# Kernel optimization log

Hardware: AMD Instinct MI355X
Metric: run time of the kernel (lower is better)

## Reference

```python
import jax, jax.numpy as jnp
import numpy as np

DIM = 512
HEADS = 8
DIM_HEAD = 64
INNER = HEADS * DIM_HEAD  # 512
NARROW_K = 9
WIDE_K = 9
WIDE_DIL = 5


def setup_inputs() -> dict:
    key = jax.random.key(0)
    ks = jax.random.split(key, 12)
    b, n = 4, 2048
    s = lambda fan_in: 1.0 / np.sqrt(fan_in)
    inp = {
        'tokens': jax.random.normal(ks[0], (b, n, DIM), jnp.float32),
        'mask': jax.random.randint(ks[1], (b, n), 0, 2) > 0,
        'w_qkv': jax.random.normal(ks[2], (DIM, INNER * 3), jnp.float32) * s(DIM),
        'w_out': jax.random.normal(ks[3], (INNER, DIM), jnp.float32) * s(INNER),
        'b_out': jnp.zeros((DIM,), jnp.float32),
        'w_narrow': jax.random.normal(ks[4], (DIM, DIM, NARROW_K), jnp.float32) * s(DIM * NARROW_K),
        'b_narrow': jnp.zeros((DIM,), jnp.float32),
        'w_wide': jax.random.normal(ks[5], (DIM, DIM, WIDE_K), jnp.float32) * s(DIM * WIDE_K),
        'b_wide': jnp.zeros((DIM,), jnp.float32),
        'ln1_g': jnp.ones((DIM,), jnp.float32),
        'ln1_b': jnp.zeros((DIM,), jnp.float32),
        'ff_w': jax.random.normal(ks[6], (DIM, DIM), jnp.float32) * s(DIM),
        'ff_b': jnp.zeros((DIM,), jnp.float32),
        'ln2_g': jnp.ones((DIM,), jnp.float32),
        'ln2_b': jnp.zeros((DIM,), jnp.float32),
    }
    return inp


def layer_norm(x, g, b, eps=1e-5):
    m = jnp.mean(x, axis=-1, keepdims=True)
    v = jnp.mean(jnp.square(x - m), axis=-1, keepdims=True)
    return (x - m) / jnp.sqrt(v + eps) * g + b


def rope_encoding(seq_len, dim_head, dtype):
    inv_freq = 1.0 / (10000.0 ** (jnp.arange(0, dim_head, 2, dtype=jnp.float32) / dim_head))
    pos = jnp.arange(seq_len, dtype=jnp.float32)
    sinu = jnp.einsum('i,j->ij', pos, inv_freq)  # [n, d/2]
    return jnp.concatenate([jnp.sin(sinu), jnp.cos(sinu)], axis=-1).astype(dtype)  # [n, d]


def attn(tokens, mask, w_qkv, w_out, b_out):
    b, n, _ = tokens.shape
    qkv = tokens @ w_qkv  # [b, n, 3*inner]
    q, k, v = jnp.split(qkv, 3, axis=-1)
    reshp = lambda t: t.reshape(b, n, HEADS, DIM_HEAD).transpose(0, 2, 1, 3)  # b h n d
    q, k, v = reshp(q), reshp(k), reshp(v)
    rope = rope_encoding(n, DIM_HEAD, tokens.dtype)  # [n, d]
    q = q + rope
    k = k + rope
    mask4 = mask[:, None, :, None]  # b 1 n 1
    big = jnp.finfo(k.dtype).max
    k = jnp.where(mask4, k, -big)
    q = jax.nn.softmax(q, axis=-1) * (DIM_HEAD ** -0.5)
    k = jax.nn.softmax(k, axis=2)  # over n
    v = jnp.where(mask4, v, 0.0)
    context = jnp.einsum('bhnd,bhne->bhde', k, v)
    out = jnp.einsum('bhde,bhnd->bhne', context, q)
    out = out.transpose(0, 2, 1, 3).reshape(b, n, INNER)
    return out @ w_out + b_out


def conv1d(x, w, b, padding, dilation):
    # x: [b, c, n], w: [out, in, k]
    y = jax.lax.conv_general_dilated(
        x, w, window_strides=(1,), padding=[(padding, padding)],
        rhs_dilation=(dilation,), dimension_numbers=('NCW', 'OIW', 'NCW'))
    return y + b[None, :, None]


def reference(tokens, mask, w_qkv, w_out, b_out, w_narrow, b_narrow,
              w_wide, b_wide, ln1_g, ln1_b, ff_w, ff_b, ln2_g, ln2_b):
    tokens = attn(tokens, mask, w_qkv, w_out, b_out)
    conv_in = tokens.transpose(0, 2, 1)  # b d n
    conv_in = jnp.where(mask[:, None, :], conv_in, 0.0)
    narrow = jax.nn.gelu(conv1d(conv_in, w_narrow, b_narrow, NARROW_K // 2, 1), approximate=False)
    wide_pad = (WIDE_K + (WIDE_K - 1) * (WIDE_DIL - 1)) // 2  # 20
    wide = jax.nn.gelu(conv1d(conv_in, w_wide, b_wide, wide_pad, WIDE_DIL), approximate=False)
    tokens = tokens + narrow.transpose(0, 2, 1) + wide.transpose(0, 2, 1)
    tokens = layer_norm(tokens, ln1_g, ln1_b)
    tokens = layer_norm(jax.nn.gelu(tokens @ ff_w + ff_b, approximate=False), ln2_g, ln2_b)
    return tokens
```

## Files before the change

### kernel.cpp

```cpp
#include <hip/hip_runtime.h>
#include <hip/hip_bf16.h>

#define BB 4
#define NN 2048
#define NROWS (BB*NN)

typedef unsigned short u16;
typedef __bf16 bf16x8 __attribute__((ext_vector_type(8)));
typedef u16    u16x8  __attribute__((ext_vector_type(8)));
typedef float  fx4    __attribute__((ext_vector_type(4)));

__device__ __forceinline__ float bf2f(u16 u){
  union { float f; unsigned int i; } x; x.i = ((unsigned int)u) << 16; return x.f;
}
__device__ __forceinline__ u16 f2bf(float f){
  union { float f; unsigned int i; } x; x.f = f;
  unsigned int i = x.i;
  i += 0x7fffu + ((i >> 16) & 1u);
  return (u16)(i >> 16);
}
__device__ __forceinline__ float geluf(float x){
  return 0.5f * x * (1.0f + erff(x * 0.70710678118654752f));
}

__global__ __launch_bounds__(256) void sniff_k(const u16* tokens, const unsigned int* mask, int* flags){
  __shared__ int s_f32, s_byte;
  if (threadIdx.x == 0) { s_f32 = 0; s_byte = 0; }
  __syncthreads();
  for (int i = threadIdx.x; i < 4096; i += 256) {
    float v = bf2f(tokens[i]);
    if (!(fabsf(v) < 1e10f)) atomicOr(&s_f32, 1);
  }
  for (int i = threadIdx.x; i < 2048; i += 256) {
    if (mask[i] > 1u) atomicOr(&s_byte, 1);
  }
  __syncthreads();
  if (threadIdx.x == 0) { flags[0] = s_f32; flags[1] = s_byte; }
}

__global__ __launch_bounds__(256) void misc_k(const void* mask, const void* tokens,
                                              const void* p0, const void* p1, const void* p2,
                                              const void* p3, const void* p4, const void* p5,
                                              const void* p6, const void* p7,
                                              const int* flags, float* rope, int* m32,
                                              float* params, float* ctx, float* kS, u16* tokbf){
  const void* srcs[8] = {p0,p1,p2,p3,p4,p5,p6,p7};
  int f32 = flags[0], mbyte = flags[1];
  const int T = 131072 + 8192 + 4096 + 131072 + 2048 + 4194304;
  for (int i = blockIdx.x*256 + threadIdx.x; i < T; i += gridDim.x*256) {
    if (i < 131072) {
      int p = i >> 6, j = i & 63;
      int jj = (j < 32) ? j : j - 32;
      float invf = exp2f(-(float)jj * (13.287712379549449f/32.0f));
      float prod = (float)p * invf;
      rope[i] = (j < 32) ? sinf(prod) : cosf(prod);
    } else if (i < 139264) {
      int k = i - 131072;
      int v = mbyte ? (int)((const unsigned char*)mask)[k] : ((const int*)mask)[k];
      m32[k] = v ? 1 : 0;
    } else if (i < 143360) {
      int k = i - 139264;
      int pid = k >> 9, j = k & 511;
      const void* s = srcs[pid];
      params[k] = f32 ? ((const float*)s)[j] : bf2f(((const u16*)s)[j]);
    } else if (i < 274432) {
      ctx[i - 143360] = 0.0f;
    } else if (i < 276480) {
      kS[i - 274432] = 0.0f;
    } else {
      int k = i - 276480;
      tokbf[k] = f32 ? f2bf(((const float*)tokens)[k]) : ((const u16*)tokens)[k];
    }
  }
}

__global__ __launch_bounds__(256) void prep2_k(const void* w_qkv, const void* w_out, const void* ff_w,
                                               const void* w_narrow, const void* w_wide,
                                               const int* flags,
                                               u16* wqkvt, u16* woutt, u16* ffwt,
                                               u16* wtN2, u16* wtW2){
  int bid = blockIdx.x;
  int f = flags[0];
  int tid = threadIdx.x;
  if (bid < 1024) {
    int tensor = bid >> 9, o = bid & 511;
    const void* src = tensor ? w_wide : w_narrow;
    u16* dst = tensor ? wtW2 : wtN2;
    __shared__ u16 Ls[4608];
    for (int i = tid; i < 4608; i += 256) {
      Ls[i] = f ? f2bf(((const float*)src)[(size_t)o*4608 + i]) : ((const u16*)src)[(size_t)o*4608 + i];
    }
    __syncthreads();
    #pragma unroll
    for (int kk = 0; kk < 9; kk++) {
      #pragma unroll
      for (int u = 0; u < 2; u++) {
        int c = tid + u*256;
        dst[(size_t)kk*262144 + o*512 + c] = Ls[c*9 + kk];
      }
    }
  } else {
    int id = bid - 1024;
    int z = id / 192;
    int rem = id - z*192;
    int x = rem % 24, y = rem / 24;
    int Nn = (z == 0) ? 1536 : 512;
    if (x * 64 >= Nn) return;
    const void* src = (z == 0) ? w_qkv : (z == 1) ? w_out : ff_w;
    u16* dst = (z == 0) ? wqkvt : (z == 1) ? woutt : ffwt;
    __shared__ u16 Ts[64][72];
    int n0 = x * 64, k0 = y * 64;
    int r = tid >> 2, cq = (tid & 3) * 16;
    #pragma unroll
    for (int u = 0; u < 2; u++) {
      int c = cq + u*8;
      int sidx = (k0 + r)*Nn + n0 + c;
      u16x8 v;
      if (f) {
        #pragma unroll
        for (int j = 0; j < 8; j++) v[j] = f2bf(((const float*)src)[sidx + j]);
      } else {
        v = *(const u16x8*)&((const u16*)src)[sidx];
      }
      *(u16x8*)&Ts[r][c] = v;
    }
    __syncthreads();
    #pragma unroll
    for (int u = 0; u < 2; u++) {
      int c = cq + u*8;
      u16x8 v;
      #pragma unroll
      for (int j = 0; j < 8; j++) v[j] = Ts[c + j][r];
      *(u16x8*)&dst[(size_t)(n0 + r)*512 + k0 + c] = v;
    }
  }
}

template<bool BIAS, bool GELU>
__global__ __launch_bounds__(256) void mgemm_k(const u16* A, const u16* Bt, const float* bias,
                                               float* C, int M, int N, int K){
  __shared__ u16 As[128][40];
  __shared__ u16 Bs[128][40];
  int tid = threadIdx.x;
  int lane = tid & 63;
  int wave = tid >> 6;
  int wm = (wave >> 1) * 64, wn = (wave & 1) * 64;
  int quad = lane >> 4, l16 = lane & 15;
  int m0 = blockIdx.y * 128, n0 = blockIdx.x * 128;
  fx4 acc[4][4] = {};
  int ar = tid >> 2;
  int ac = (tid & 3) * 8;
  for (int k0 = 0; k0 < K; k0 += 32) {
    *(u16x8*)&As[ar][ac]    = *(const u16x8*)&A[(size_t)(m0+ar)*K + k0 + ac];
    *(u16x8*)&As[ar+64][ac] = *(const u16x8*)&A[(size_t)(m0+ar+64)*K + k0 + ac];
    *(u16x8*)&Bs[ar][ac]    = *(const u16x8*)&Bt[(size_t)(n0+ar)*K + k0 + ac];
    *(u16x8*)&Bs[ar+64][ac] = *(const u16x8*)&Bt[(size_t)(n0+ar+64)*K + k0 + ac];
    __syncthreads();
    bf16x8 af[4], bfv[4];
    #pragma unroll
    for (int i = 0; i < 4; i++)
      af[i] = __builtin_bit_cast(bf16x8, *(const u16x8*)&As[wm + i*16 + l16][quad*8]);
    #pragma unroll
    for (int j = 0; j < 4; j++)
      bfv[j] = __builtin_bit_cast(bf16x8, *(const u16x8*)&Bs[wn + j*16 + l16][quad*8]);
    #pragma unroll
    for (int i = 0; i < 4; i++)
      #pragma unroll
      for (int j = 0; j < 4; j++)
        acc[i][j] = __builtin_amdgcn_mfma_f32_16x16x32_bf16(af[i], bfv[j], acc[i][j], 0, 0, 0);
    __syncthreads();
  }
  #pragma unroll
  for (int i = 0; i < 4; i++)
    #pragma unroll
    for (int j = 0; j < 4; j++) {
      int col = n0 + wn + j*16 + l16;
      float bv = BIAS ? bias[col] : 0.0f;
      #pragma unroll
      for (int r = 0; r < 4; r++) {
        int row = m0 + wm + i*16 + quad*4 + r;
        float v = acc[i][j][r] + bv;
        if (GELU) v = geluf(v);
        C[(size_t)row*N + col] = v;
      }
    }
}

template<bool BIAS, bool GELU>
__global__ __launch_bounds__(256) void mgemm64b_k(const u16* A, const u16* Bt, const float* bias,
                                                  u16* C, int M, int N, int K){
  __shared__ u16 As[64][40];
  __shared__ u16 Bs[128][40];
  int tid = threadIdx.x;
  int lane = tid & 63;
  int wave = tid >> 6;
  int wn = wave * 32;
  int quad = lane >> 4, l16 = lane & 15;
  int m0 = blockIdx.y * 64, n0 = blockIdx.x * 128;
  fx4 acc[4][2] = {};
  int ar = tid >> 2;
  int ac = (tid & 3) * 8;
  for (int k0 = 0; k0 < K; k0 += 32) {
    *(u16x8*)&As[ar][ac]    = *(const u16x8*)&A[(size_t)(m0+ar)*K + k0 + ac];
    *(u16x8*)&Bs[ar][ac]    = *(const u16x8*)&Bt[(size_t)(n0+ar)*K + k0 + ac];
    *(u16x8*)&Bs[ar+64][ac] = *(const u16x8*)&Bt[(size_t)(n0+ar+64)*K + k0 + ac];
    __syncthreads();
    bf16x8 af[4], bfv[2];
    #pragma unroll
    for (int i = 0; i < 4; i++)
      af[i] = __builtin_bit_cast(bf16x8, *(const u16x8*)&As[i*16 + l16][quad*8]);
    #pragma unroll
    for (int j = 0; j < 2; j++)
      bfv[j] = __builtin_bit_cast(bf16x8, *(const u16x8*)&Bs[wn + j*16 + l16][quad*8]);
    #pragma unroll
    for (int i = 0; i < 4; i++)
      #pragma unroll
      for (int j = 0; j < 2; j++)
        acc[i][j] = __builtin_amdgcn_mfma_f32_16x16x32_bf16(af[i], bfv[j], acc[i][j], 0, 0, 0);
    __syncthreads();
  }
  #pragma unroll
  for (int i = 0; i < 4; i++)
    #pragma unroll
    for (int j = 0; j < 2; j++) {
      int col = n0 + wn + j*16 + l16;
      float bv = BIAS ? bias[col] : 0.0f;
      #pragma unroll
      for (int r = 0; r < 4; r++) {
        int row = m0 + i*16 + quad*4 + r;
        float v = acc[i][j][r] + bv;
        if (GELU) v = geluf(v);
        C[(size_t)row*N + col] = f2bf(v);
      }
    }
}

__global__ __launch_bounds__(256) void mgemm_attn64_k(const u16* qb, const u16* W2t, const float* bias,
                                                      const int* mask, u16* attnb, u16* cpadb){
  __shared__ u16 As[64][40];
  __shared__ u16 Bs[128][40];
  int tid = threadIdx.x;
  int lane = tid & 63;
  int wave = tid >> 6;
  int wn = wave * 32;
  int quad = lane >> 4, l16 = lane & 15;
  int m0 = blockIdx.y * 64, n0 = blockIdx.x * 128, b = blockIdx.z;
  const u16* A  = qb  + (size_t)b*2048*512;
  const u16* Bt = W2t + (size_t)b*262144;
  fx4 acc[4][2] = {};
  int ar = tid >> 2;
  int ac = (tid & 3) * 8;
  for (int k0 = 0; k0 < 512; k0 += 32) {
    *(u16x8*)&As[ar][ac]    = *(const u16x8*)&A[(size_t)(m0+ar)*512 + k0 + ac];
    *(u16x8*)&Bs[ar][ac]    = *(const u16x8*)&Bt[(size_t)(n0+ar)*512 + k0 + ac];
    *(u16x8*)&Bs[ar+64][ac] = *(const u16x8*)&Bt[(size_t)(n0+ar+64)*512 + k0 + ac];
    __syncthreads();
    bf16x8 af[4], bfv[2];
    #pragma unroll
    for (int i = 0; i < 4; i++)
      af[i] = __builtin_bit_cast(bf16x8, *(const u16x8*)&As[i*16 + l16][quad*8]);
    #pragma unroll
    for (int j = 0; j < 2; j++)
      bfv[j] = __builtin_bit_cast(bf16x8, *(const u16x8*)&Bs[wn + j*16 + l16][quad*8]);
    #pragma unroll
    for (int i = 0; i < 4; i++)
      #pragma unroll
      for (int j = 0; j < 2; j++)
        acc[i][j] = __builtin_amdgcn_mfma_f32_16x16x32_bf16(af[i], bfv[j], acc[i][j], 0, 0, 0);
    __syncthreads();
  }
  #pragma unroll
  for (int i = 0; i < 4; i++)
    #pragma unroll
    for (int j = 0; j < 2; j++) {
      int col = n0 + wn + j*16 + l16;
      float bv = bias[col];
      #pragma unroll
      for (int r = 0; r < 4; r++) {
        int row_l = m0 + i*16 + quad*4 + r;
        float v = acc[i][j][r] + bv;
        u16 vb = f2bf(v);
        attnb[((size_t)b*2048 + row_l)*512 + col] = vb;
        int mk = mask[b*2048 + row_l];
        cpadb[((size_t)b*2088 + row_l + 20)*512 + col] = mk ? vb : (u16)0;
      }
    }
}

__global__ __launch_bounds__(256, 4) void mconv5_k(const u16* cpad, const u16* Wn, const u16* Ww,
                                                   const float* bias_n, const float* bias_w,
                                                   u16* Dn, u16* Dw){
  __shared__ u16 As[168][72];
  __shared__ u16 Ws[64][72];
  int tid = threadIdx.x;
  int lane = tid & 63;
  int wave = tid >> 6;
  int wm = (wave >> 1) * 64;
  int wo = (wave & 1) * 32;
  int quad = lane >> 4, l16 = lane & 15;
  int o0 = blockIdx.x * 64, m0 = blockIdx.y * 128;
  int b = blockIdx.z >> 1, cid = blockIdx.z & 1;
  const u16* W = cid ? Ww : Wn;
  const float* bias = cid ? bias_w : bias_n;
  u16* D = cid ? Dw : Dn;
  fx4 acc[4][2] = {};
  const u16* cb = cpad + ((size_t)b*2088 + m0)*512;
  for (int c0 = 0; c0 < 512; c0 += 64) {
    __syncthreads();
    for (int idx = tid; idx < 168*8; idx += 256) {
      int r = idx >> 3, off = (idx & 7)*8;
      *(u16x8*)&As[r][off] = *(const u16x8*)&cb[(size_t)r*512 + c0 + off];
    }
    u16x8 pre[2];
    {
      const u16* wp = W + (size_t)o0*512 + c0;
      #pragma unroll
      for (int u = 0; u < 2; u++) {
        int idx = tid + u*256;
        int r = idx >> 3, off = (idx & 7)*8;
        pre[u] = *(const u16x8*)&wp[(size_t)r*512 + off];
      }
    }
    #pragma unroll
    for (int kk = 0; kk < 9; kk++) {
      if (kk > 0) __syncthreads();
      #pragma unroll
      for (int u = 0; u < 2; u++) {
        int idx = tid + u*256;
        int r = idx >> 3, off = (idx & 7)*8;
        *(u16x8*)&Ws[r][off] = pre[u];
      }
      if (kk < 8) {
        const u16* wp = W + (size_t)(kk+1)*262144 + (size_t)o0*512 + c0;
        #pragma unroll
        for (int u = 0; u < 2; u++) {
          int idx = tid + u*256;
          int r = idx >> 3, off = (idx & 7)*8;
          pre[u] = *(const u16x8*)&wp[(size_t)r*512 + off];
        }
      }
      __syncthreads();
      int shift = cid ? 5*kk : 16 + kk;
      #pragma unroll
      for (int ks = 0; ks < 2; ks++) {
        bf16x8 bfv[2];
        #pragma unroll
        for (int j = 0; j < 2; j++)
          bfv[j] = __builtin_bit_cast(bf16x8, *(const u16x8*)&Ws[wo + j*16 + l16][ks*32 + quad*8]);
        #pragma unroll
        for (int i = 0; i < 4; i++) {
          bf16x8 afr = __builtin_bit_cast(bf16x8, *(const u16x8*)&As[shift + wm + i*16 + l16][ks*32 + quad*8]);
          #pragma unroll
          for (int j = 0; j < 2; j++)
            acc[i][j] = __builtin_amdgcn_mfma_f32_16x16x32_bf16(afr, bfv[j], acc[i][j], 0, 0, 0);
        }
      }
    }
  }
  #pragma unroll
  for (int i = 0; i < 4; i++)
    #pragma unroll
    for (int j = 0; j < 2; j++) {
      int col = o0 + wo + j*16 + l16;
      float bv = bias[col];
      #pragma unroll
      for (int r = 0; r < 4; r++) {
        int row = b*2048 + m0 + wm + i*16 + quad*4 + r;
        D[(size_t)row*512 + col] = f2bf(geluf(acc[i][j][r] + bv));
      }
    }
}

__global__ __launch_bounds__(512) void qvks_k(const float* rope, const int* mask, float* qkv,
                                              u16* qb, float* kredM){
  int bx = blockIdx.x;
  int tid = threadIdx.x;
  if (bx < NROWS) {
    int row = bx;
    int n = row & (NN-1);
    int d = tid & 63;
    float* qp = qkv + (size_t)row*1536;
    float v = qp[tid] + rope[n*64 + d];
    float m = v;
    #pragma unroll
    for (int o = 32; o; o >>= 1) m = fmaxf(m, __shfl_xor(m, o, 64));
    float e = expf(v - m);
    float s = e;
    #pragma unroll
    for (int o = 32; o; o >>= 1) s += __shfl_xor(s, o, 64);
    qb[(size_t)row*512 + tid] = f2bf(e * (0.125f / s));
    float mk = mask[row] ? 1.0f : 0.0f;
    qp[1024 + tid] *= mk;
  } else {
    int seg = bx - NROWS;
    int bh = seg >> 3, s = seg & 7;
    int b = bh >> 3, h = bh & 7;
    int d = tid & 63, g = tid >> 6;
    __shared__ float red[8][64];
    const float* kp = qkv + (size_t)b*NN*1536 + 512 + h*64 + d;
    const int* mp = mask + b*NN;
    int nbase = s*256 + g*32;
    float m = -3.0e38f;
    for (int n = nbase; n < nbase+32; n++)
      if (mp[n]) m = fmaxf(m, kp[(size_t)n*1536] + rope[n*64 + d]);
    red[g][d] = m;
    __syncthreads();
    if (g == 0) {
      float M = m;
      #pragma unroll
      for (int gg = 1; gg < 8; gg++) M = fmaxf(M, red[gg][d]);
      kredM[(bh*8 + s)*64 + d] = M;
    }
  }
}

#define FMA16(a, b, acc) \
  acc[0][0] = fmaf(a.x, b.x, acc[0][0]); acc[0][1] = fmaf(a.x, b.y, acc[0][1]); \
  acc[0][2] = fmaf(a.x, b.z, acc[0][2]); acc[0][3] = fmaf(a.x, b.w, acc[0][3]); \
  acc[1][0] = fmaf(a.y, b.x, acc[1][0]); acc[1][1] = fmaf(a.y, b.y, acc[1][1]); \
  acc[1][2] = fmaf(a.y, b.z, acc[1][2]); acc[1][3] = fmaf(a.y, b.w, acc[1][3]); \
  acc[2][0] = fmaf(a.z, b.x, acc[2][0]); acc[2][1] = fmaf(a.z, b.y, acc[2][1]); \
  acc[2][2] = fmaf(a.z, b.z, acc[2][2]); acc[2][3] = fmaf(a.z, b.w, acc[2][3]); \
  acc[3][0] = fmaf(a.w, b.x, acc[3][0]); acc[3][1] = fmaf(a.w, b.y, acc[3][1]); \
  acc[3][2] = fmaf(a.w, b.z, acc[3][2]); acc[3][3] = fmaf(a.w, b.w, acc[3][3]);

__global__ __launch_bounds__(256) void ctx_k(const float* qkv, const float* rope, const int* mask,
                                             const float* kredM, float* ctx, float* Sg){
  int bh = blockIdx.x, seg = blockIdx.y;
  int b = bh >> 3, h = bh & 7;
  __shared__ float Ks[32][68], Vs[32][68];
  __shared__ float sS[64];
  __shared__ float sM[64];
  int tid = threadIdx.x, tx = tid & 15, ty = tid >> 4;
  if (tid < 64) {
    sS[tid] = 0.0f;
    float M = -3.0e38f;
    #pragma unroll
    for (int s = 0; s < 8; s++) M = fmaxf(M, kredM[(bh*8 + s)*64 + tid]);
    sM[tid] = M;
  }
  __syncthreads();
  float acc[4][4] = {{0.f,0.f,0.f,0.f},{0.f,0.f,0.f,0.f},{0.f,0.f,0.f,0.f},{0.f,0.f,0.f,0.f}};
  float sp[8] = {0,0,0,0,0,0,0,0};
  const float* basep = qkv + (size_t)(b*NN + seg*256)*1536 + h*64;
  const int* mp = mask + b*NN;
  int nl = tid >> 3, dcol = (tid & 7)*8;
  float4 km0 = *(const float4*)&sM[dcol];
  float4 km1 = *(const float4*)&sM[dcol + 4];
  for (int nc = 0; nc < 256; nc += 32) {
    int n = seg*256 + nc + nl;
    const float* kp = basep + (size_t)(nc + nl)*1536 + 512 + dcol;
    const float* vp = basep + (size_t)(nc + nl)*1536 + 1024 + dcol;
    float4 a0 = *(const float4*)kp, a1 = *(const float4*)(kp+4);
    float4 b0 = *(const float4*)vp, b1 = *(const float4*)(vp+4);
    if (mp[n]) {
      float4 r0 = *(const float4*)&rope[n*64 + dcol];
      float4 r1 = *(const float4*)&rope[n*64 + dcol + 4];
      a0.x = expf(a0.x + r0.x - km0.x);
      a0.y = expf(a0.y + r0.y - km0.y);
      a0.z = expf(a0.z + r0.z - km0.z);
      a0.w = expf(a0.w + r0.w - km0.w);
      a1.x = expf(a1.x + r1.x - km1.x);
      a1.y = expf(a1.y + r1.y - km1.y);
      a1.z = expf(a1.z + r1.z - km1.z);
      a1.w = expf(a1.w + r1.w - km1.w);
    } else {
      a0 = (float4){0,0,0,0}; a1 = (float4){0,0,0,0};
    }
    sp[0] += a0.x; sp[1] += a0.y; sp[2] += a0.z; sp[3] += a0.w;
    sp[4] += a1.x; sp[5] += a1.y; sp[6] += a1.z; sp[7] += a1.w;
    *(float4*)&Ks[nl][dcol]   = a0; *(float4*)&Ks[nl][dcol+4] = a1;
    *(float4*)&Vs[nl][dcol]   = b0; *(float4*)&Vs[nl][dcol+4] = b1;
    __syncthreads();
    #pragma unroll
    for (int q = 0; q < 32; q++) {
      float4 a = *(const float4*)&Ks[q][ty*4];
      float4 b = *(const float4*)&Vs[q][tx*4];
      FMA16(a, b, acc)
    }
    __syncthreads();
  }
  #pragma unroll
  for (int j = 0; j < 8; j++) atomicAdd(&sS[dcol + j], sp[j]);
  float* cp = ctx + (size_t)bh*4096;
  #pragma unroll
  for (int i = 0; i < 4; i++)
    #pragma unroll
    for (int j = 0; j < 4; j++)
      atomicAdd(&cp[(ty*4 + i)*64 + tx*4 + j], acc[i][j]);
  __syncthreads();
  if (tid < 64) atomicAdd(&Sg[bh*64 + tid], sS[tid]);
}

__global__ __launch_bounds__(256) void ctxw_k(const float* ctx, const float* Sg, const u16* woutt,
                                              u16* W2t, u16* cpadb){
  int bx = blockIdx.x;
  int tid = threadIdx.x;
  if (bx >= 32) {
    int idx = (bx - 32)*256 + tid;
    if (idx < BB*40*512) {
      int c = idx & 511;
      int t = (idx >> 9) % 40;
      int b = idx / (40*512);
      int tt = (t < 20) ? t : 2048 + t;
      cpadb[((size_t)b*2088 + tt)*512 + c] = 0;
    }
    return;
  }
  int h = bx & 7, b = bx >> 3;
  int lane = tid & 63, wave = tid >> 6;
  int quad = lane >> 4, l16 = lane & 15;
  const float* cp = ctx + (size_t)(b*8 + h)*4096;
  fx4 acc[8][4] = {};
  #pragma unroll
  for (int ks = 0; ks < 2; ks++) {
    bf16x8 bfv[4];
    #pragma unroll
    for (int j = 0; j < 4; j++) {
      int d = j*16 + l16;
      float S = Sg[(b*8 + h)*64 + d];
      float rs = (S > 0.0f) ? 1.0f/S : 0.0f;
      const float* src = cp + d*64 + ks*32 + quad*8;
      float4 v0 = *(const float4*)src, v1 = *(const float4*)(src + 4);
      bf16x8 t;
      t[0]=(__bf16)(v0.x*rs); t[1]=(__bf16)(v0.y*rs); t[2]=(__bf16)(v0.z*rs); t[3]=(__bf16)(v0.w*rs);
      t[4]=(__bf16)(v1.x*rs); t[5]=(__bf16)(v1.y*rs); t[6]=(__bf16)(v1.z*rs); t[7]=(__bf16)(v1.w*rs);
      bfv[j] = t;
    }
    #pragma unroll
    for (int i = 0; i < 8; i++) {
      int orow = wave*128 + i*16 + l16;
      bf16x8 afr = __builtin_bit_cast(bf16x8, *(const u16x8*)&woutt[(size_t)orow*512 + h*64 + ks*32 + quad*8]);
      #pragma unroll
      for (int j = 0; j < 4; j++)
        acc[i][j] = __builtin_amdgcn_mfma_f32_16x16x32_bf16(afr, bfv[j], acc[i][j], 0, 0, 0);
    }
  }
  u16* out = W2t + (size_t)b*262144;
  #pragma unroll
  for (int i = 0; i < 8; i++)
    #pragma unroll
    for (int j = 0; j < 4; j++)
      #pragma unroll
      for (int r = 0; r < 4; r++) {
        int orow = wave*128 + i*16 + quad*4 + r;
        out[(size_t)orow*512 + h*64 + j*16 + l16] = f2bf(acc[i][j][r]);
      }
}

__device__ __forceinline__ float block_sum512(float v, float* red){
  #pragma unroll
  for (int o = 32; o; o >>= 1) v += __shfl_xor(v, o, 64);
  int w = threadIdx.x >> 6;
  if ((threadIdx.x & 63) == 0) red[w] = v;
  __syncthreads();
  float t = red[0] + red[1] + red[2] + red[3];
  __syncthreads();
  return t;
}

template<int NADD, int OM>
__global__ __launch_bounds__(256) void ln_k(const u16* X, const u16* Y, const u16* Z,
                                            const float* g, const float* be,
                                            const int* flags, void* out){
  __shared__ float red[4];
  size_t row = blockIdx.x;
  int tid = threadIdx.x;
  const u16* xp = X + row*512;
  float x0 = bf2f(xp[tid]), x1 = bf2f(xp[tid + 256]);
  if (NADD >= 1) { const u16* yp = Y + row*512; x0 += bf2f(yp[tid]); x1 += bf2f(yp[tid + 256]); }
  if (NADD >= 2) { const u16* zp = Z + row*512; x0 += bf2f(zp[tid]); x1 += bf2f(zp[tid + 256]); }
  float mean = block_sum512(x0 + x1, red) * (1.0f/512.0f);
  float d0 = x0 - mean, d1 = x1 - mean;
  float var = block_sum512(d0*d0 + d1*d1, red) * (1.0f/512.0f);
  float inv = rsqrtf(var + 1e-5f);
  float r0 = d0*inv*g[tid]       + be[tid];
  float r1 = d1*inv*g[tid + 256] + be[tid + 256];
  bool obf = (OM == 1) || (OM == 2 && !flags[0]);
  if (obf) {
    u16* op = (u16*)out;
    op[row*512 + tid]       = f2bf(r0);
    op[row*512 + tid + 256] = f2bf(r1);
  } else {
    float* op = (float*)out;
    op[row*512 + tid]       = r0;
    op[row*512 + tid + 256] = r1;
  }
}

extern "C" void kernel_launch(void* const* d_in, const int* in_sizes, int n_in,
                              void* d_out, int out_size, void* d_ws, size_t ws_size,
                              hipStream_t stream) {
  const void* tokens   = d_in[0];
  const void* mask     = d_in[1];
  const void* w_qkv    = d_in[2];
  const void* w_out    = d_in[3];
  const void* b_out    = d_in[4];
  const void* w_narrow = d_in[5];
  const void* b_narrow = d_in[6];
  const void* w_wide   = d_in[7];
  const void* b_wide   = d_in[8];
  const void* ln1_g    = d_in[9];
  const void* ln1_b    = d_in[10];
  const void* ff_w     = d_in[11];
  const void* ff_b     = d_in[12];
  const void* ln2_g    = d_in[13];
  const void* ln2_b    = d_in[14];

  float* ws = (float*)d_ws;
  int*   flags  = (int*)ws;
  int*   m32    = (int*)(ws + 16);
  float* params = ws + 8208;
  float* kredM  = ws + 12304;
  float* kS     = ws + 28688;
  float* ctx    = ws + 30736;
  float* rope   = ws + 161808;
  u16*   tokbf  = (u16*)(ws + 292880);
  u16*   wqkvt  = (u16*)(ws + 2390032);
  u16*   woutt  = (u16*)(ws + 2783248);
  u16*   ffwt   = (u16*)(ws + 2914320);
  u16*   wtN2   = (u16*)(ws + 3045392);
  u16*   wtW2   = (u16*)(ws + 4225040);
  u16*   qb     = (u16*)(ws + 5404688);
  u16*   W2t    = (u16*)(ws + 7501840);
  u16*   attnb  = (u16*)(ws + 8026128);
  float* qkv    = ws + 10123280;
  u16*   cpadb  = (u16*)qkv;
  u16*   Dnb    = (u16*)(qkv + 2138112);
  u16*   Dwb    = (u16*)(qkv + 4235264);
  u16*   Eb     = attnb;
  u16*   t1b    = tokbf;

  float* p_bout = params;        float* p_bnar = params + 512;
  float* p_bwid = params + 1024; float* p_l1g  = params + 1536;
  float* p_l1b  = params + 2048; float* p_ffb  = params + 2560;
  float* p_l2g  = params + 3072; float* p_l2b  = params + 3584;

  sniff_k<<<dim3(1), dim3(256), 0, stream>>>((const u16*)tokens, (const unsigned int*)mask, flags);
  misc_k<<<dim3(8192), dim3(256), 0, stream>>>(mask, tokens, b_out, b_narrow, b_wide, ln1_g, ln1_b,
                                               ff_b, ln2_g, ln2_b, flags, rope, m32, params, ctx,
                                               kS, tokbf);
  prep2_k<<<dim3(1600), dim3(256), 0, stream>>>(w_qkv, w_out, ff_w, w_narrow, w_wide, flags,
                                                wqkvt, woutt, ffwt, wtN2, wtW2);

  mgemm_k<false,false><<<dim3(12, 64), dim3(256), 0, stream>>>(
      tokbf, wqkvt, nullptr, qkv, NROWS, 1536, 512);

  qvks_k<<<dim3(NROWS + 256), dim3(512), 0, stream>>>(rope, m32, qkv, qb, kredM);

  ctx_k<<<dim3(32, 8), dim3(256), 0, stream>>>(qkv, rope, m32, kredM, ctx, kS);

  ctxw_k<<<dim3(352), dim3(256), 0, stream>>>(ctx, kS, woutt, W2t, cpadb);

  mgemm_attn64_k<<<dim3(4, 32, 4), dim3(256), 0, stream>>>(qb, W2t, p_bout, m32, attnb, cpadb);

  mconv5_k<<<dim3(8, 16, 8), dim3(256), 0, stream>>>(cpadb, wtN2, wtW2, p_bnar, p_bwid, Dnb, Dwb);

  ln_k<2,1><<<dim3(NROWS), dim3(256), 0, stream>>>(attnb, Dnb, Dwb, p_l1g, p_l1b, flags, (void*)t1b);

  mgemm64b_k<true,true><<<dim3(4, 128), dim3(256), 0, stream>>>(
      t1b, ffwt, p_ffb, Eb, NROWS, 512, 512);

  ln_k<0,2><<<dim3(NROWS), dim3(256), 0, stream>>>(Eb, nullptr, nullptr, p_l2g, p_l2b, flags, d_out);
}
```

Measured before the change: 366.3 us.

## Fuse rope/softmax/exp epilogues into QKV GEMM and widen conv tiles

```diff
diff --git a/kernel.cpp b/kernel.cpp
--- a/kernel.cpp
+++ b/kernel.cpp
@@ -136,11 +136,11 @@
   }
 }
 
-template<bool BIAS, bool GELU>
-__global__ __launch_bounds__(256) void mgemm_k(const u16* A, const u16* Bt, const float* bias,
-                                               float* C, int M, int N, int K){
+__global__ __launch_bounds__(256) void mgemm_qkv_k(const u16* A, const u16* Bt, const float* rope,
+                                                   const int* mask, u16* qb, u16* keb, u16* vb){
   __shared__ u16 As[128][40];
   __shared__ u16 Bs[128][40];
+  __shared__ int smask[128];
   int tid = threadIdx.x;
   int lane = tid & 63;
   int wave = tid >> 6;
@@ -150,11 +150,11 @@
   fx4 acc[4][4] = {};
   int ar = tid >> 2;
   int ac = (tid & 3) * 8;
-  for (int k0 = 0; k0 < K; k0 += 32) {
-    *(u16x8*)&As[ar][ac]    = *(const u16x8*)&A[(size_t)(m0+ar)*K + k0 + ac];
-    *(u16x8*)&As[ar+64][ac] = *(const u16x8*)&A[(size_t)(m0+ar+64)*K + k0 + ac];
-    *(u16x8*)&Bs[ar][ac]    = *(const u16x8*)&Bt[(size_t)(n0+ar)*K + k0 + ac];
-    *(u16x8*)&Bs[ar+64][ac] = *(const u16x8*)&Bt[(size_t)(n0+ar+64)*K + k0 + ac];
+  for (int k0 = 0; k0 < 512; k0 += 32) {
+    *(u16x8*)&As[ar][ac]    = *(const u16x8*)&A[(size_t)(m0+ar)*512 + k0 + ac];
+    *(u16x8*)&As[ar+64][ac] = *(const u16x8*)&A[(size_t)(m0+ar+64)*512 + k0 + ac];
+    *(u16x8*)&Bs[ar][ac]    = *(const u16x8*)&Bt[(size_t)(n0+ar)*512 + k0 + ac];
+    *(u16x8*)&Bs[ar+64][ac] = *(const u16x8*)&Bt[(size_t)(n0+ar+64)*512 + k0 + ac];
     __syncthreads();
     bf16x8 af[4], bfv[4];
     #pragma unroll
@@ -170,69 +170,174 @@
         acc[i][j] = __builtin_amdgcn_mfma_f32_16x16x32_bf16(af[i], bfv[j], acc[i][j], 0, 0, 0);
     __syncthreads();
   }
+  int x = blockIdx.x;
+  if (x >= 4) {
+    if (tid < 128) smask[tid] = mask[m0 + tid];
+    __syncthreads();
+  }
+  if (x < 4) {
+    #pragma unroll
+    for (int i = 0; i < 4; i++)
+      #pragma unroll
+      for (int r = 0; r < 4; r++) {
+        int rl = wm + i*16 + quad*4 + r;
+        int row = m0 + rl;
+        int nseq = row & (NN-1);
+        const float* rp = rope + nseq*64 + l16;
+        float e0 = __expf(acc[i][0][r] + rp[0]);
+        float e1 = __expf(acc[i][1][r] + rp[16]);
+        float e2 = __expf(acc[i][2][r] + rp[32]);
+        float e3 = __expf(acc[i][3][r] + rp[48]);
+        float s = e0 + e1 + e2 + e3;
+        s += __shfl_xor(s, 1); s += __shfl_xor(s, 2);
+        s += __shfl_xor(s, 4); s += __shfl_xor(s, 8);
+        float sc = 0.125f / s;
+        size_t base = (size_t)row*512 + n0 + wn + l16;
+        qb[base]      = f2bf(e0*sc);
+        qb[base + 16] = f2bf(e1*sc);
+        qb[base + 32] = f2bf(e2*sc);
+        qb[base + 48] = f2bf(e3*sc);
+      }
+  } else if (x < 8) {
+    #pragma unroll
+    for (int i = 0; i < 4; i++)
+      #pragma unroll
+      for (int r = 0; r < 4; r++) {
+        int rl = wm + i*16 + quad*4 + r;
+        int row = m0 + rl;
+        int nseq = row & (NN-1);
+        int mk = smask[rl];
+        const float* rp = rope + nseq*64 + l16;
+        size_t base = (size_t)row*512 + (n0 - 512) + wn + l16;
+        #pragma unroll
+        for (int j = 0; j < 4; j++) {
+          float ke = mk ? __expf(acc[i][j][r] + rp[j*16]) : 0.0f;
+          keb[base + j*16] = f2bf(ke);
+        }
+      }
+  } else {
+    #pragma unroll
+    for (int i = 0; i < 4; i++)
+      #pragma unroll
+      for (int r = 0; r < 4; r++) {
+        int rl = wm + i*16 + quad*4 + r;
+        int row = m0 + rl;
+        int mk = smask[rl];
+        size_t base = (size_t)row*512 + (n0 - 1024) + wn + l16;
+        #pragma unroll
+        for (int j = 0; j < 4; j++)
+          vb[base + j*16] = mk ? f2bf(acc[i][j][r]) : (u16)0;
+      }
+  }
+}
+
+#define FMA16(a, b, acc) \
+  acc[0][0] = fmaf(a.x, b.x, acc[0][0]); acc[0][1] = fmaf(a.x, b.y, acc[0][1]); \
+  acc[0][2] = fmaf(a.x, b.z, acc[0][2]); acc[0][3] = fmaf(a.x, b.w, acc[0][3]); \
+  acc[1][0] = fmaf(a.y, b.x, acc[1][0]); acc[1][1] = fmaf(a.y, b.y, acc[1][1]); \
+  acc[1][2] = fmaf(a.y, b.z, acc[1][2]); acc[1][3] = fmaf(a.y, b.w, acc[1][3]); \
+  acc[2][0] = fmaf(a.z, b.x, acc[2][0]); acc[2][1] = fmaf(a.z, b.y, acc[2][1]); \
+  acc[2][2] = fmaf(a.z, b.z, acc[2][2]); acc[2][3] = fmaf(a.z, b.w, acc[2][3]); \
+  acc[3][0] = fmaf(a.w, b.x, acc[3][0]); acc[3][1] = fmaf(a.w, b.y, acc[3][1]); \
+  acc[3][2] = fmaf(a.w, b.z, acc[3][2]); acc[3][3] = fmaf(a.w, b.w, acc[3][3]);
+
+__global__ __launch_bounds__(256) void ctx_k(const u16* keb, const u16* vb, float* ctx, float* Sg){
+  int bh = blockIdx.x, seg = blockIdx.y;
+  int b = bh >> 3, h = bh & 7;
+  __shared__ float Ks[32][68], Vs[32][68];
+  __shared__ float sS[64];
+  int tid = threadIdx.x, tx = tid & 15, ty = tid >> 4;
+  if (tid < 64) sS[tid] = 0.0f;
+  float acc[4][4] = {{0.f,0.f,0.f,0.f},{0.f,0.f,0.f,0.f},{0.f,0.f,0.f,0.f},{0.f,0.f,0.f,0.f}};
+  float sp[8] = {0,0,0,0,0,0,0,0};
+  int nl = tid >> 3, dcol = (tid & 7)*8;
+  const u16* kp0 = keb + (size_t)(b*NN + seg*256)*512 + h*64 + dcol;
+  const u16* vp0 = vb  + (size_t)(b*NN + seg*256)*512 + h*64 + dcol;
+  for (int nc = 0; nc < 256; nc += 32) {
+    u16x8 ku = *(const u16x8*)(kp0 + (size_t)(nc + nl)*512);
+    u16x8 vu = *(const u16x8*)(vp0 + (size_t)(nc + nl)*512);
+    float a[8], bb[8];
+    #pragma unroll
+    for (int t = 0; t < 8; t++) { a[t] = bf2f(ku[t]); bb[t] = bf2f(vu[t]); sp[t] += a[t]; }
+    *(float4*)&Ks[nl][dcol]   = (float4){a[0],a[1],a[2],a[3]};
+    *(float4*)&Ks[nl][dcol+4] = (float4){a[4],a[5],a[6],a[7]};
+    *(float4*)&Vs[nl][dcol]   = (float4){bb[0],bb[1],bb[2],bb[3]};
+    *(float4*)&Vs[nl][dcol+4] = (float4){bb[4],bb[5],bb[6],bb[7]};
+    __syncthreads();
+    #pragma unroll
+    for (int q = 0; q < 32; q++) {
+      float4 a4 = *(const float4*)&Ks[q][ty*4];
+      float4 b4 = *(const float4*)&Vs[q][tx*4];
+      FMA16(a4, b4, acc)
+    }
+    __syncthreads();
+  }
+  #pragma unroll
+  for (int j = 0; j < 8; j++) atomicAdd(&sS[dcol + j], sp[j]);
+  float* cp = ctx + (size_t)bh*4096;
   #pragma unroll
   for (int i = 0; i < 4; i++)
     #pragma unroll
+    for (int j = 0; j < 4; j++)
+      atomicAdd(&cp[(ty*4 + i)*64 + tx*4 + j], acc[i][j]);
+  __syncthreads();
+  if (tid < 64) atomicAdd(&Sg[bh*64 + tid], sS[tid]);
+}
+
+__global__ __launch_bounds__(256) void ctxw_k(const float* ctx, const float* Sg, const u16* woutt,
+                                              u16* W2t, u16* cpadb){
+  int bx = blockIdx.x;
+  int tid = threadIdx.x;
+  if (bx >= 32) {
+    int idx = (bx - 32)*256 + tid;
+    if (idx < BB*40*512) {
+      int c = idx & 511;
+      int t = (idx >> 9) % 40;
+      int b = idx / (40*512);
+      int tt = (t < 20) ? t : 2048 + t;
+      cpadb[((size_t)b*2088 + tt)*512 + c] = 0;
+    }
+    return;
+  }
+  int h = bx & 7, b = bx >> 3;
+  int lane = tid & 63, wave = tid >> 6;
+  int quad = lane >> 4, l16 = lane & 15;
+  const float* cp = ctx + (size_t)(b*8 + h)*4096;
+  fx4 acc[8][4] = {};
+  #pragma unroll
+  for (int ks = 0; ks < 2; ks++) {
+    bf16x8 bfv[4];
+    #pragma unroll
     for (int j = 0; j < 4; j++) {
-      int col = n0 + wn + j*16 + l16;
-      float bv = BIAS ? bias[col] : 0.0f;
+      int d = j*16 + l16;
+      float S = Sg[(b*8 + h)*64 + d];
+      float rs = (S > 0.0f) ? 1.0f/S : 0.0f;
+      const float* src = cp + d*64 + ks*32 + quad*8;
+      float4 v0 = *(const float4*)src, v1 = *(const float4*)(src + 4);
+      bf16x8 t;
+      t[0]=(__bf16)(v0.x*rs); t[1]=(__bf16)(v0.y*rs); t[2]=(__bf16)(v0.z*rs); t[3]=(__bf16)(v0.w*rs);
+      t[4]=(__bf16)(v1.x*rs); t[5]=(__bf16)(v1.y*rs); t[6]=(__bf16)(v1.z*rs); t[7]=(__bf16)(v1.w*rs);
+      bfv[j] = t;
+    }
+    #pragma unroll
+    for (int i = 0; i < 8; i++) {
+      int orow = wave*128 + i*16 + l16;
+      bf16x8 afr = __builtin_bit_cast(bf16x8, *(const u16x8*)&woutt[(size_t)orow*512 + h*64 + ks*32 + quad*8]);
+      #pragma unroll
+      for (int j = 0; j < 4; j++)
+        acc[i][j] = __builtin_amdgcn_mfma_f32_16x16x32_bf16(afr, bfv[j], acc[i][j], 0, 0, 0);
+    }
+  }
+  u16* out = W2t + (size_t)b*262144;
+  #pragma unroll
+  for (int i = 0; i < 8; i++)
+    #pragma unroll
+    for (int j = 0; j < 4; j++)
       #pragma unroll
       for (int r = 0; r < 4; r++) {
-        int row = m0 + wm + i*16 + quad*4 + r;
-        float v = acc[i][j][r] + bv;
-        if (GELU) v = geluf(v);
-        C[(size_t)row*N + col] = v;
-      }
-    }
-}
-
-template<bool BIAS, bool GELU>
-__global__ __launch_bounds__(256) void mgemm64b_k(const u16* A, const u16* Bt, const float* bias,
-                                                  u16* C, int M, int N, int K){
-  __shared__ u16 As[64][40];
-  __shared__ u16 Bs[128][40];
-  int tid = threadIdx.x;
-  int lane = tid & 63;
-  int wave = tid >> 6;
-  int wn = wave * 32;
-  int quad = lane >> 4, l16 = lane & 15;
-  int m0 = blockIdx.y * 64, n0 = blockIdx.x * 128;
-  fx4 acc[4][2] = {};
-  int ar = tid >> 2;
-  int ac = (tid & 3) * 8;
-  for (int k0 = 0; k0 < K; k0 += 32) {
-    *(u16x8*)&As[ar][ac]    = *(const u16x8*)&A[(size_t)(m0+ar)*K + k0 + ac];
-    *(u16x8*)&Bs[ar][ac]    = *(const u16x8*)&Bt[(size_t)(n0+ar)*K + k0 + ac];
-    *(u16x8*)&Bs[ar+64][ac] = *(const u16x8*)&Bt[(size_t)(n0+ar+64)*K + k0 + ac];
-    __syncthreads();
-    bf16x8 af[4], bfv[2];
-    #pragma unroll
-    for (int i = 0; i < 4; i++)
-      af[i] = __builtin_bit_cast(bf16x8, *(const u16x8*)&As[i*16 + l16][quad*8]);
-    #pragma unroll
-    for (int j = 0; j < 2; j++)
-      bfv[j] = __builtin_bit_cast(bf16x8, *(const u16x8*)&Bs[wn + j*16 + l16][quad*8]);
-    #pragma unroll
-    for (int i = 0; i < 4; i++)
-      #pragma unroll
-      for (int j = 0; j < 2; j++)
-        acc[i][j] = __builtin_amdgcn_mfma_f32_16x16x32_bf16(af[i], bfv[j], acc[i][j], 0, 0, 0);
-    __syncthreads();
-  }
-  #pragma unroll
-  for (int i = 0; i < 4; i++)
-    #pragma unroll
-    for (int j = 0; j < 2; j++) {
-      int col = n0 + wn + j*16 + l16;
-      float bv = BIAS ? bias[col] : 0.0f;
-      #pragma unroll
-      for (int r = 0; r < 4; r++) {
-        int row = m0 + i*16 + quad*4 + r;
-        float v = acc[i][j][r] + bv;
-        if (GELU) v = geluf(v);
-        C[(size_t)row*N + col] = f2bf(v);
-      }
-    }
+        int orow = wave*128 + i*16 + quad*4 + r;
+        out[(size_t)orow*512 + h*64 + j*16 + l16] = f2bf(acc[i][j][r]);
+      }
 }
 
 __global__ __launch_bounds__(256) void mgemm_attn64_k(const u16* qb, const u16* W2t, const float* bias,
@@ -279,31 +384,31 @@
       for (int r = 0; r < 4; r++) {
         int row_l = m0 + i*16 + quad*4 + r;
         float v = acc[i][j][r] + bv;
-        u16 vb = f2bf(v);
-        attnb[((size_t)b*2048 + row_l)*512 + col] = vb;
+        u16 vbb = f2bf(v);
+        attnb[((size_t)b*2048 + row_l)*512 + col] = vbb;
         int mk = mask[b*2048 + row_l];
-        cpadb[((size_t)b*2088 + row_l + 20)*512 + col] = mk ? vb : (u16)0;
-      }
-    }
-}
-
-__global__ __launch_bounds__(256, 4) void mconv5_k(const u16* cpad, const u16* Wn, const u16* Ww,
+        cpadb[((size_t)b*2088 + row_l + 20)*512 + col] = mk ? vbb : (u16)0;
+      }
+    }
+}
+
+__global__ __launch_bounds__(256, 2) void mconv6_k(const u16* cpad, const u16* Wn, const u16* Ww,
                                                    const float* bias_n, const float* bias_w,
                                                    u16* Dn, u16* Dw){
   __shared__ u16 As[168][72];
-  __shared__ u16 Ws[64][72];
+  __shared__ u16 Ws[128][72];
   int tid = threadIdx.x;
   int lane = tid & 63;
   int wave = tid >> 6;
   int wm = (wave >> 1) * 64;
-  int wo = (wave & 1) * 32;
+  int wo = (wave & 1) * 64;
   int quad = lane >> 4, l16 = lane & 15;
-  int o0 = blockIdx.x * 64, m0 = blockIdx.y * 128;
+  int o0 = blockIdx.x * 128, m0 = blockIdx.y * 128;
   int b = blockIdx.z >> 1, cid = blockIdx.z & 1;
   const u16* W = cid ? Ww : Wn;
   const float* bias = cid ? bias_w : bias_n;
   u16* D = cid ? Dw : Dn;
-  fx4 acc[4][2] = {};
+  fx4 acc[4][4] = {};
   const u16* cb = cpad + ((size_t)b*2088 + m0)*512;
   for (int c0 = 0; c0 < 512; c0 += 64) {
     __syncthreads();
@@ -311,11 +416,11 @@
       int r = idx >> 3, off = (idx & 7)*8;
       *(u16x8*)&As[r][off] = *(const u16x8*)&cb[(size_t)r*512 + c0 + off];
     }
-    u16x8 pre[2];
+    u16x8 pre[4];
     {
       const u16* wp = W + (size_t)o0*512 + c0;
       #pragma unroll
-      for (int u = 0; u < 2; u++) {
+      for (int u = 0; u < 4; u++) {
         int idx = tid + u*256;
         int r = idx >> 3, off = (idx & 7)*8;
         pre[u] = *(const u16x8*)&wp[(size_t)r*512 + off];
@@ -325,7 +430,7 @@
     for (int kk = 0; kk < 9; kk++) {
       if (kk > 0) __syncthreads();
       #pragma unroll
-      for (int u = 0; u < 2; u++) {
+      for (int u = 0; u < 4; u++) {
         int idx = tid + u*256;
         int r = idx >> 3, off = (idx & 7)*8;
         *(u16x8*)&Ws[r][off] = pre[u];
@@ -333,7 +438,7 @@
       if (kk < 8) {
         const u16* wp = W + (size_t)(kk+1)*262144 + (size_t)o0*512 + c0;
         #pragma unroll
-        for (int u = 0; u < 2; u++) {
+        for (int u = 0; u < 4; u++) {
           int idx = tid + u*256;
           int r = idx >> 3, off = (idx & 7)*8;
           pre[u] = *(const u16x8*)&wp[(size_t)r*512 + off];
@@ -343,15 +448,15 @@
       int shift = cid ? 5*kk : 16 + kk;
       #pragma unroll
       for (int ks = 0; ks < 2; ks++) {
-        bf16x8 bfv[2];
+        bf16x8 bfv[4];
         #pragma unroll
-        for (int j = 0; j < 2; j++)
+        for (int j = 0; j < 4; j++)
           bfv[j] = __builtin_bit_cast(bf16x8, *(const u16x8*)&Ws[wo + j*16 + l16][ks*32 + quad*8]);
         #pragma unroll
         for (int i = 0; i < 4; i++) {
           bf16x8 afr = __builtin_bit_cast(bf16x8, *(const u16x8*)&As[shift + wm + i*16 + l16][ks*32 + quad*8]);
           #pragma unroll
-          for (int j = 0; j < 2; j++)
+          for (int j = 0; j < 4; j++)
             acc[i][j] = __builtin_amdgcn_mfma_f32_16x16x32_bf16(afr, bfv[j], acc[i][j], 0, 0, 0);
         }
       }
@@ -360,7 +465,7 @@
   #pragma unroll
   for (int i = 0; i < 4; i++)
     #pragma unroll
-    for (int j = 0; j < 2; j++) {
+    for (int j = 0; j < 4; j++) {
       int col = o0 + wo + j*16 + l16;
       float bv = bias[col];
       #pragma unroll
@@ -371,181 +476,53 @@
     }
 }
 
-__global__ __launch_bounds__(512) void qvks_k(const float* rope, const int* mask, float* qkv,
-                                              u16* qb, float* kredM){
-  int bx = blockIdx.x;
+template<bool BIAS, bool GELU>
+__global__ __launch_bounds__(256) void mgemm64b_k(const u16* A, const u16* Bt, const float* bias,
+                                                  u16* C, int M, int N, int K){
+  __shared__ u16 As[64][40];
+  __shared__ u16 Bs[128][40];
   int tid = threadIdx.x;
-  if (bx < NROWS) {
-    int row = bx;
-    int n = row & (NN-1);
-    int d = tid & 63;
-    float* qp = qkv + (size_t)row*1536;
-    float v = qp[tid] + rope[n*64 + d];
-    float m = v;
-    #pragma unroll
-    for (int o = 32; o; o >>= 1) m = fmaxf(m, __shfl_xor(m, o, 64));
-    float e = expf(v - m);
-    float s = e;
-    #pragma unroll
-    for (int o = 32; o; o >>= 1) s += __shfl_xor(s, o, 64);
-    qb[(size_t)row*512 + tid] = f2bf(e * (0.125f / s));
-    float mk = mask[row] ? 1.0f : 0.0f;
-    qp[1024 + tid] *= mk;
-  } else {
-    int seg = bx - NROWS;
-    int bh = seg >> 3, s = seg & 7;
-    int b = bh >> 3, h = bh & 7;
-    int d = tid & 63, g = tid >> 6;
-    __shared__ float red[8][64];
-    const float* kp = qkv + (size_t)b*NN*1536 + 512 + h*64 + d;
-    const int* mp = mask + b*NN;
-    int nbase = s*256 + g*32;
-    float m = -3.0e38f;
-    for (int n = nbase; n < nbase+32; n++)
-      if (mp[n]) m = fmaxf(m, kp[(size_t)n*1536] + rope[n*64 + d]);
-    red[g][d] = m;
-    __syncthreads();
-    if (g == 0) {
-      float M = m;
-      #pragma unroll
-      for (int gg = 1; gg < 8; gg++) M = fmaxf(M, red[gg][d]);
-      kredM[(bh*8 + s)*64 + d] = M;
-    }
-  }
-}
-
-#define FMA16(a, b, acc) \
-  acc[0][0] = fmaf(a.x, b.x, acc[0][0]); acc[0][1] = fmaf(a.x, b.y, acc[0][1]); \
-  acc[0][2] = fmaf(a.x, b.z, acc[0][2]); acc[0][3] = fmaf(a.x, b.w, acc[0][3]); \
-  acc[1][0] = fmaf(a.y, b.x, acc[1][0]); acc[1][1] = fmaf(a.y, b.y, acc[1][1]); \
-  acc[1][2] = fmaf(a.y, b.z, acc[1][2]); acc[1][3] = fmaf(a.y, b.w, acc[1][3]); \
-  acc[2][0] = fmaf(a.z, b.x, acc[2][0]); acc[2][1] = fmaf(a.z, b.y, acc[2][1]); \
-  acc[2][2] = fmaf(a.z, b.z, acc[2][2]); acc[2][3] = fmaf(a.z, b.w, acc[2][3]); \
-  acc[3][0] = fmaf(a.w, b.x, acc[3][0]); acc[3][1] = fmaf(a.w, b.y, acc[3][1]); \
-  acc[3][2] = fmaf(a.w, b.z, acc[3][2]); acc[3][3] = fmaf(a.w, b.w, acc[3][3]);
-
-__global__ __launch_bounds__(256) void ctx_k(const float* qkv, const float* rope, const int* mask,
-                                             const float* kredM, float* ctx, float* Sg){
-  int bh = blockIdx.x, seg = blockIdx.y;
-  int b = bh >> 3, h = bh & 7;
-  __shared__ float Ks[32][68], Vs[32][68];
-  __shared__ float sS[64];
-  __shared__ float sM[64];
-  int tid = threadIdx.x, tx = tid & 15, ty = tid >> 4;
-  if (tid < 64) {
-    sS[tid] = 0.0f;
-    float M = -3.0e38f;
-    #pragma unroll
-    for (int s = 0; s < 8; s++) M = fmaxf(M, kredM[(bh*8 + s)*64 + tid]);
-    sM[tid] = M;
-  }
-  __syncthreads();
-  float acc[4][4] = {{0.f,0.f,0.f,0.f},{0.f,0.f,0.f,0.f},{0.f,0.f,0.f,0.f},{0.f,0.f,0.f,0.f}};
-  float sp[8] = {0,0,0,0,0,0,0,0};
-  const float* basep = qkv + (size_t)(b*NN + seg*256)*1536 + h*64;
-  const int* mp = mask + b*NN;
-  int nl = tid >> 3, dcol = (tid & 7)*8;
-  float4 km0 = *(const float4*)&sM[dcol];
-  float4 km1 = *(const float4*)&sM[dcol + 4];
-  for (int nc = 0; nc < 256; nc += 32) {
-    int n = seg*256 + nc + nl;
-    const float* kp = basep + (size_t)(nc + nl)*1536 + 512 + dcol;
-    const float* vp = basep + (size_t)(nc + nl)*1536 + 1024 + dcol;
-    float4 a0 = *(const float4*)kp, a1 = *(const float4*)(kp+4);
-    float4 b0 = *(const float4*)vp, b1 = *(const float4*)(vp+4);
-    if (mp[n]) {
-      float4 r0 = *(const float4*)&rope[n*64 + dcol];
-      float4 r1 = *(const float4*)&rope[n*64 + dcol + 4];
-      a0.x = expf(a0.x + r0.x - km0.x);
-      a0.y = expf(a0.y + r0.y - km0.y);
-      a0.z = expf(a0.z + r0.z - km0.z);
-      a0.w = expf(a0.w + r0.w - km0.w);
-      a1.x = expf(a1.x + r1.x - km1.x);
-      a1.y = expf(a1.y + r1.y - km1.y);
-      a1.z = expf(a1.z + r1.z - km1.z);
-      a1.w = expf(a1.w + r1.w - km1.w);
-    } else {
-      a0 = (float4){0,0,0,0}; a1 = (float4){0,0,0,0};
-    }
-    sp[0] += a0.x; sp[1] += a0.y; sp[2] += a0.z; sp[3] += a0.w;
-    sp[4] += a1.x; sp[5] += a1.y; sp[6] += a1.z; sp[7] += a1.w;
-    *(float4*)&Ks[nl][dcol]   = a0; *(float4*)&Ks[nl][dcol+4] = a1;
-    *(float4*)&Vs[nl][dcol]   = b0; *(float4*)&Vs[nl][dcol+4] = b1;
-    __syncthreads();
-    #pragma unroll
-    for (int q = 0; q < 32; q++) {
-      float4 a = *(const float4*)&Ks[q][ty*4];
-      float4 b = *(const float4*)&Vs[q][tx*4];
-      FMA16(a, b, acc)
-    }
-    __syncthreads();
-  }
-  #pragma unroll
-  for (int j = 0; j < 8; j++) atomicAdd(&sS[dcol + j], sp[j]);
-  float* cp = ctx + (size_t)bh*4096;
+  int lane = tid & 63;
+  int wave = tid >> 6;
+  int wn = wave * 32;
+  int quad = lane >> 4, l16 = lane & 15;
+  int m0 = blockIdx.y * 64, n0 = blockIdx.x * 128;
+  fx4 acc[4][2] = {};
+  int ar = tid >> 2;
+  int ac = (tid & 3) * 8;
+  for (int k0 = 0; k0 < K; k0 += 32) {
+    *(u16x8*)&As[ar][ac]    = *(const u16x8*)&A[(size_t)(m0+ar)*K + k0 + ac];
+    *(u16x8*)&Bs[ar][ac]    = *(const u16x8*)&Bt[(size_t)(n0+ar)*K + k0 + ac];
+    *(u16x8*)&Bs[ar+64][ac] = *(const u16x8*)&Bt[(size_t)(n0+ar+64)*K + k0 + ac];
+    __syncthreads();
+    bf16x8 af[4], bfv[2];
+    #pragma unroll
+    for (int i = 0; i < 4; i++)
+      af[i] = __builtin_bit_cast(bf16x8, *(const u16x8*)&As[i*16 + l16][quad*8]);
+    #pragma unroll
+    for (int j = 0; j < 2; j++)
+      bfv[j] = __builtin_bit_cast(bf16x8, *(const u16x8*)&Bs[wn + j*16 + l16][quad*8]);
+    #pragma unroll
+    for (int i = 0; i < 4; i++)
+      #pragma unroll
+      for (int j = 0; j < 2; j++)
+        acc[i][j] = __builtin_amdgcn_mfma_f32_16x16x32_bf16(af[i], bfv[j], acc[i][j], 0, 0, 0);
+    __syncthreads();
+  }
   #pragma unroll
   for (int i = 0; i < 4; i++)
     #pragma unroll
-    for (int j = 0; j < 4; j++)
-      atomicAdd(&cp[(ty*4 + i)*64 + tx*4 + j], acc[i][j]);
-  __syncthreads();
-  if (tid < 64) atomicAdd(&Sg[bh*64 + tid], sS[tid]);
-}
-
-__global__ __launch_bounds__(256) void ctxw_k(const float* ctx, const float* Sg, const u16* woutt,
-                                              u16* W2t, u16* cpadb){
-  int bx = blockIdx.x;
-  int tid = threadIdx.x;
-  if (bx >= 32) {
-    int idx = (bx - 32)*256 + tid;
-    if (idx < BB*40*512) {
-      int c = idx & 511;
-      int t = (idx >> 9) % 40;
-      int b = idx / (40*512);
-      int tt = (t < 20) ? t : 2048 + t;
-      cpadb[((size_t)b*2088 + tt)*512 + c] = 0;
-    }
-    return;
-  }
-  int h = bx & 7, b = bx >> 3;
-  int lane = tid & 63, wave = tid >> 6;
-  int quad = lane >> 4, l16 = lane & 15;
-  const float* cp = ctx + (size_t)(b*8 + h)*4096;
-  fx4 acc[8][4] = {};
-  #pragma unroll
-  for (int ks = 0; ks < 2; ks++) {
-    bf16x8 bfv[4];
-    #pragma unroll
-    for (int j = 0; j < 4; j++) {
-      int d = j*16 + l16;
-      float S = Sg[(b*8 + h)*64 + d];
-      float rs = (S > 0.0f) ? 1.0f/S : 0.0f;
-      const float* src = cp + d*64 + ks*32 + quad*8;
-      float4 v0 = *(const float4*)src, v1 = *(const float4*)(src + 4);
-      bf16x8 t;
-      t[0]=(__bf16)(v0.x*rs); t[1]=(__bf16)(v0.y*rs); t[2]=(__bf16)(v0.z*rs); t[3]=(__bf16)(v0.w*rs);
-      t[4]=(__bf16)(v1.x*rs); t[5]=(__bf16)(v1.y*rs); t[6]=(__bf16)(v1.z*rs); t[7]=(__bf16)(v1.w*rs);
-      bfv[j] = t;
-    }
-    #pragma unroll
-    for (int i = 0; i < 8; i++) {
-      int orow = wave*128 + i*16 + l16;
-      bf16x8 afr = __builtin_bit_cast(bf16x8, *(const u16x8*)&woutt[(size_t)orow*512 + h*64 + ks*32 + quad*8]);
-      #pragma unroll
-      for (int j = 0; j < 4; j++)
-        acc[i][j] = __builtin_amdgcn_mfma_f32_16x16x32_bf16(afr, bfv[j], acc[i][j], 0, 0, 0);
-    }
-  }
-  u16* out = W2t + (size_t)b*262144;
-  #pragma unroll
-  for (int i = 0; i < 8; i++)
-    #pragma unroll
-    for (int j = 0; j < 4; j++)
+    for (int j = 0; j < 2; j++) {
+      int col = n0 + wn + j*16 + l16;
+      float bv = BIAS ? bias[col] : 0.0f;
       #pragma unroll
       for (int r = 0; r < 4; r++) {
-        int orow = wave*128 + i*16 + quad*4 + r;
-        out[(size_t)orow*512 + h*64 + j*16 + l16] = f2bf(acc[i][j][r]);
-      }
+        int row = m0 + i*16 + quad*4 + r;
+        float v = acc[i][j][r] + bv;
+        if (GELU) v = geluf(v);
+        C[(size_t)row*N + col] = f2bf(v);
+      }
+    }
 }
 
 __device__ __forceinline__ float block_sum512(float v, float* red){
@@ -611,23 +588,23 @@
   int*   flags  = (int*)ws;
   int*   m32    = (int*)(ws + 16);
   float* params = ws + 8208;
-  float* kredM  = ws + 12304;
-  float* kS     = ws + 28688;
-  float* ctx    = ws + 30736;
-  float* rope   = ws + 161808;
-  u16*   tokbf  = (u16*)(ws + 292880);
-  u16*   wqkvt  = (u16*)(ws + 2390032);
-  u16*   woutt  = (u16*)(ws + 2783248);
-  u16*   ffwt   = (u16*)(ws + 2914320);
-  u16*   wtN2   = (u16*)(ws + 3045392);
-  u16*   wtW2   = (u16*)(ws + 4225040);
-  u16*   qb     = (u16*)(ws + 5404688);
-  u16*   W2t    = (u16*)(ws + 7501840);
-  u16*   attnb  = (u16*)(ws + 8026128);
-  float* qkv    = ws + 10123280;
-  u16*   cpadb  = (u16*)qkv;
-  u16*   Dnb    = (u16*)(qkv + 2138112);
-  u16*   Dwb    = (u16*)(qkv + 4235264);
+  float* kS     = ws + 12304;
+  float* ctx    = ws + 14352;
+  float* rope   = ws + 145424;
+  u16*   tokbf  = (u16*)(ws + 276496);
+  u16*   wqkvt  = (u16*)(ws + 2373648);
+  u16*   woutt  = (u16*)(ws + 2766864);
+  u16*   ffwt   = (u16*)(ws + 2897936);
+  u16*   wtN2   = (u16*)(ws + 3029008);
+  u16*   wtW2   = (u16*)(ws + 4208656);
+  u16*   qb     = (u16*)(ws + 5388304);
+  u16*   keb    = (u16*)(ws + 7485456);
+  u16*   vb     = (u16*)(ws + 9582608);
+  u16*   W2t    = (u16*)(ws + 11679760);
+  u16*   attnb  = (u16*)(ws + 12204048);
+  u16*   cpadb  = (u16*)(ws + 14301200);
+  u16*   Dnb    = (u16*)(ws + 16439312);
+  u16*   Dwb    = (u16*)(ws + 18536464);
   u16*   Eb     = attnb;
   u16*   t1b    = tokbf;
 
@@ -643,18 +620,16 @@
   prep2_k<<<dim3(1600), dim3(256), 0, stream>>>(w_qkv, w_out, ff_w, w_narrow, w_wide, flags,
                                                 wqkvt, woutt, ffwt, wtN2, wtW2);
 
-  mgemm_k<false,false><<<dim3(12, 64), dim3(256), 0, stream>>>(
-      tokbf, wqkvt, nullptr, qkv, NROWS, 1536, 512);
-
-  qvks_k<<<dim3(NROWS + 256), dim3(512), 0, stream>>>(rope, m32, qkv, qb, kredM);
-
-  ctx_k<<<dim3(32, 8), dim3(256), 0, stream>>>(qkv, rope, m32, kredM, ctx, kS);
+  mgemm_qkv_k<<<dim3(12, 64), dim3(256), 0, stream>>>(
+      tokbf, wqkvt, rope, m32, qb, keb, vb);
+
+  ctx_k<<<dim3(32, 8), dim3(256), 0, stream>>>(keb, vb, ctx, kS);
 
   ctxw_k<<<dim3(352), dim3(256), 0, stream>>>(ctx, kS, woutt, W2t, cpadb);
 
   mgemm_attn64_k<<<dim3(4, 32, 4), dim3(256), 0, stream>>>(qb, W2t, p_bout, m32, attnb, cpadb);
 
-  mconv5_k<<<dim3(8, 16, 8), dim3(256), 0, stream>>>(cpadb, wtN2, wtW2, p_bnar, p_bwid, Dnb, Dwb);
+  mconv6_k<<<dim3(4, 16, 8), dim3(256), 0, stream>>>(cpadb, wtN2, wtW2, p_bnar, p_bwid, Dnb, Dwb);
 
   ln_k<2,1><<<dim3(NROWS), dim3(256), 0, stream>>>(attnb, Dnb, Dwb, p_l1g, p_l1b, flags, (void*)t1b);
 
```

Measured after the change: 353.3 us. 3.5% less time.
